# Performance work log

Measured on AMD Instinct MI355X. Metric: run time of the kernel, lower is better.

## Reference

```python
import jax, jax.numpy as jnp
import numpy as np

N_NODES = 100000
N_EDGES = 1600000
IN_FEATS, HIDDEN, N_CLASSES = 128, 64, 16


def setup_inputs() -> dict:
    key = jax.random.key(0)
    ks = jax.random.split(key, 10)
    feats = jax.random.normal(ks[0], (N_NODES, IN_FEATS), dtype=jnp.float32)
    src = jax.random.randint(ks[1], (N_EDGES,), 0, N_NODES, dtype=jnp.int32)
    dst = jax.random.randint(ks[2], (N_EDGES,), 0, N_NODES, dtype=jnp.int32)
    def glorot(k, fan_in, fan_out):
        lim = np.sqrt(6.0 / (fan_in + fan_out)).astype(np.float32)
        return jax.random.uniform(k, (fan_in, fan_out), jnp.float32, -lim, lim)
    return {
        "features": feats, "src": src, "dst": dst,
        "W0": glorot(ks[3], IN_FEATS, HIDDEN), "b0": jnp.zeros((HIDDEN,), jnp.float32),
        "W1": glorot(ks[4], HIDDEN, HIDDEN), "b1": jnp.zeros((HIDDEN,), jnp.float32),
        "W2": glorot(ks[5], HIDDEN, N_CLASSES), "b2": jnp.zeros((N_CLASSES,), jnp.float32),
    }


def _graph_conv(src, dst, x, W, b, act):
    # DGL GraphConv, norm='both': out = D_in^{-1/2} A (D_out^{-1/2} x) W + b
    n = x.shape[0]
    ones = jnp.ones((src.shape[0],), x.dtype)
    deg_out = jnp.clip(jax.ops.segment_sum(ones, src, num_segments=n), 1.0)
    deg_in = jnp.clip(jax.ops.segment_sum(ones, dst, num_segments=n), 1.0)
    # DGL applies W first when in_dim > out_dim (same math, less edge traffic)
    pre = x.shape[1] > W.shape[1]
    h = x @ W if pre else x
    h = h * jax.lax.rsqrt(deg_out)[:, None]
    agg = jax.ops.segment_sum(h[src], dst, num_segments=n)  # [N, d]
    agg = agg * jax.lax.rsqrt(deg_in)[:, None]
    out = (agg if pre else agg @ W) + b
    return act(out) if act is not None else out


def reference(features, src, dst, W0, b0, W1, b1, W2, b2):
    relu = jax.nn.relu
    h = _graph_conv(src, dst, features, W0, b0, relu)
    h = _graph_conv(src, dst, h, W1, b1, relu)        # dropout p=0.0 -> identity
    h = _graph_conv(src, dst, h, W2, b2, None)
    return h
```

## Files before the change

### kernel.cpp

```cpp
#include <hip/hip_runtime.h>

#define NN 100000
#define NE 1600000
#define NBUCK 782
#define PCHUNK 4096
#define HISTB 256
#define NREP 8
#define STAGE_CAP 12288

struct alignas(8) US4 { unsigned short x, y, z, w; };

__device__ __forceinline__ float bfu(unsigned int hw) { return __uint_as_float(hw << 16); }
__device__ __forceinline__ unsigned short f2bf(float f) {
    unsigned int u = __float_as_uint(f);
    return (unsigned short)((u + 0x7fffu + ((u >> 16) & 1u)) >> 16);
}


__global__ __launch_bounds__(256) void k_hist(const int* __restrict__ src,
                                              const int* __restrict__ dst,
                                              int* __restrict__ bcnt8_d,
                                              int* __restrict__ bcnt8_s) {
    __shared__ int hd[NBUCK], hs[NBUCK];
    int tid = threadIdx.x;
    for (int i = tid; i < NBUCK; i += 256) { hd[i] = 0; hs[i] = 0; }
    __syncthreads();
    int* md = bcnt8_d + (size_t)(blockIdx.x & (NREP - 1)) * NBUCK;
    int* ms = bcnt8_s + (size_t)(blockIdx.x & (NREP - 1)) * NBUCK;
    int stride = gridDim.x * 256;
    for (int e = blockIdx.x * 256 + tid; e < NE; e += stride) {
        atomicAdd(&hd[dst[e] >> 7], 1);
        atomicAdd(&hs[src[e] >> 7], 1);
    }
    __syncthreads();
    for (int i = tid; i < NBUCK; i += 256) {
        if (hd[i]) atomicAdd(&md[i], hd[i]);
        if (hs[i]) atomicAdd(&ms[i], hs[i]);
    }
}

__global__ __launch_bounds__(1024) void k_bscan(const int* __restrict__ bcnt8_d,
                                                const int* __restrict__ bcnt8_s,
                                                int* __restrict__ base_d,
                                                int* __restrict__ cursor_d,
                                                int* __restrict__ base_s,
                                                int* __restrict__ cursor_s,
                                                unsigned short* __restrict__ A,
                                                unsigned short* __restrict__ B,
                                                unsigned short* __restrict__ C16,
                                                int* __restrict__ EBg) {
    if (blockIdx.x == 2) {
        int t = threadIdx.x;
        if (t < 64) {
            A[(size_t)NN * 64 + t] = 0;
            B[(size_t)NN * 64 + t] = 0;
        }
        if (t < 16) {
            C16[(size_t)NN * 16 + t] = 0;
            EBg[NE + t] = NN;
        }
        return;
    }
    __shared__ int tmp[1024];
    int t = threadIdx.x;
    const int* bc = blockIdx.x ? bcnt8_s : bcnt8_d;
    int* base = blockIdx.x ? base_s : base_d;
    int* cur = blockIdx.x ? cursor_s : cursor_d;
    int v = 0;
    if (t < NBUCK)
#pragma unroll
        for (int c = 0; c < NREP; ++c) v += bc[c * NBUCK + t];
    tmp[t] = v;
    __syncthreads();
    for (int off = 1; off < 1024; off <<= 1) {
        int u = (t >= off) ? tmp[t - off] : 0;
        __syncthreads();
        tmp[t] += u;
        __syncthreads();
    }
    int excl = tmp[t] - v;
    if (t < NBUCK) {
        base[t] = excl;
        cur[t] = excl;
    }
    if (t == 0) base[NBUCK] = NE;
}

__global__ __launch_bounds__(256) void k_pairs(const int* __restrict__ src,
                                               const int* __restrict__ dst,
                                               int* __restrict__ cursor_d,
                                               int* __restrict__ cursor_s,
                                               int* __restrict__ E2d,
                                               unsigned char* __restrict__ E2s) {
    __shared__ int hist_d[NBUCK], gbase_d[NBUCK], hist_s[NBUCK], gbase_s[NBUCK];
    int tid = threadIdx.x;
    for (int i = tid; i < NBUCK; i += 256) { hist_d[i] = 0; hist_s[i] = 0; }
    __syncthreads();
    int base = blockIdx.x * PCHUNK;
#pragma unroll
    for (int i = 0; i < PCHUNK / 256; ++i) {
        int e = base + i * 256 + tid;
        if (e < NE) {
            atomicAdd(&hist_d[dst[e] >> 7], 1);
            atomicAdd(&hist_s[src[e] >> 7], 1);
        }
    }
    __syncthreads();
    int rot = (int)((blockIdx.x * 191u) % NBUCK);
    for (int ii = tid; ii < NBUCK; ii += 256) {
        int i = ii + rot;
        if (i >= NBUCK) i -= NBUCK;
        int h = hist_d[i];
        if (h) gbase_d[i] = atomicAdd(&cursor_d[i], h);
        hist_d[i] = 0;
        h = hist_s[i];
        if (h) gbase_s[i] = atomicAdd(&cursor_s[i], h);
        hist_s[i] = 0;
    }
    __syncthreads();
#pragma unroll
    for (int i = 0; i < PCHUNK / 256; ++i) {
        int e = base + i * 256 + tid;
        if (e < NE) {
            int s = src[e], d = dst[e];
            int bd = d >> 7;
            int pd = atomicAdd(&hist_d[bd], 1);
            E2d[gbase_d[bd] + pd] = (s << 7) | (d & 127);
            int bs = s >> 7;
            int ps = atomicAdd(&hist_s[bs], 1);
            E2s[gbase_s[bs] + ps] = (unsigned char)(s & 127);
        }
    }
}

__global__ __launch_bounds__(256) void k_nodes(int* __restrict__ EB,
                                               const int* __restrict__ base_d,
                                               const unsigned char* __restrict__ E2s,
                                               const int* __restrict__ base_s,
                                               int* __restrict__ rowdesc,
                                               float* __restrict__ r_in,
                                               float* __restrict__ r_out) {
    __shared__ int cnt[128], cur[128];
    __shared__ int stage[STAGE_CAP];
    int tid = threadIdx.x;
    int b = blockIdx.x;
    if (b >= NBUCK) {
        b -= NBUCK;
        int base = base_s[b], end = base_s[b + 1];
        if (tid < 128) cnt[tid] = 0;
        __syncthreads();
        for (int i = base + tid; i < end; i += 256) atomicAdd(&cnt[E2s[i]], 1);
        __syncthreads();
        if (tid < 128) {
            int node = b * 128 + tid;
            if (node < NN) r_out[node] = rsqrtf((float)max(cnt[tid], 1));
        }
        return;
    }
    int base = base_d[b], end = base_d[b + 1];
    int m = min(end - base, STAGE_CAP);
    if (tid < 128) cnt[tid] = 0;
    __syncthreads();
    for (int i = tid; i < m; i += 256) {
        int e = EB[base + i];
        stage[i] = e;
        atomicAdd(&cnt[e & 127], 1);
    }
    __syncthreads();
    int v = (tid < 128) ? cnt[tid] : 0;
    for (int off = 1; off < 128; off <<= 1) {
        int u = (tid >= off && tid < 128) ? cnt[tid - off] : 0;
        __syncthreads();
        if (tid < 128) cnt[tid] += u;
        __syncthreads();
    }
    if (tid < 128) {
        int excl = cnt[tid] - v;
        cur[tid] = excl;
        int node = b * 128 + tid;
        if (node < NN) {
            rowdesc[node] = ((base + excl) << 9) | min(v, 511);
            r_in[node] = rsqrtf((float)max(v, 1));
        }
    }
    __syncthreads();
    for (int i = tid; i < m; i += 256) {
        int e = stage[i];
        int pos = atomicAdd(&cur[e & 127], 1);
        EB[base + pos] = e >> 7;
    }
}


__global__ __launch_bounds__(256) void k_gemm0(const float* __restrict__ x,
                                               const float* __restrict__ W0,
                                               const float* __restrict__ r_out,
                                               unsigned short* __restrict__ A) {
    __shared__ float xl[64 * 129];
    __shared__ float wl[64 * 64];
    int tid = threadIdx.x;
    int m0 = blockIdx.x * 64;
#pragma unroll
    for (int i = 0; i < 8; ++i) {
        int idx = i * 256 + tid;
        int m = idx >> 5, kc = idx & 31;
        int gm = min(m0 + m, NN - 1);
        float4 v = *(const float4*)&x[(size_t)gm * 128 + kc * 4];
        float* p = &xl[m * 129 + kc * 4];
        p[0] = v.x; p[1] = v.y; p[2] = v.z; p[3] = v.w;
    }
    int tn = tid & 15, tm = tid >> 4;
    float acc[4][4] = {};
    const float4* W4 = (const float4*)W0;
    float4* wl4 = (float4*)wl;
    for (int h = 0; h < 2; ++h) {
        __syncthreads();
#pragma unroll
        for (int i = 0; i < 4; ++i) wl4[i * 256 + tid] = W4[h * 1024 + i * 256 + tid];
        __syncthreads();
#pragma unroll 4
        for (int k = 0; k < 64; ++k) {
            int kk = h * 64 + k;
            float4 wv = *(const float4*)&wl[k * 64 + tn * 4];
            float xv[4];
#pragma unroll
            for (int i = 0; i < 4; ++i) xv[i] = xl[(tm * 4 + i) * 129 + kk];
#pragma unroll
            for (int i = 0; i < 4; ++i) {
                acc[i][0] = fmaf(xv[i], wv.x, acc[i][0]);
                acc[i][1] = fmaf(xv[i], wv.y, acc[i][1]);
                acc[i][2] = fmaf(xv[i], wv.z, acc[i][2]);
                acc[i][3] = fmaf(xv[i], wv.w, acc[i][3]);
            }
        }
    }
#pragma unroll
    for (int i = 0; i < 4; ++i) {
        int m = m0 + tm * 4 + i;
        if (m < NN) {
            float ro = r_out[m];
            US4 o = {f2bf(acc[i][0] * ro), f2bf(acc[i][1] * ro),
                     f2bf(acc[i][2] * ro), f2bf(acc[i][3] * ro)};
            *(US4*)&A[(size_t)m * 64 + tn * 4] = o;
        }
    }
}

__global__ __launch_bounds__(256) void k_mlp(const unsigned short* __restrict__ G,
                                             const float* __restrict__ W1,
                                             const float* __restrict__ b1,
                                             const float* __restrict__ W2,
                                             const float* __restrict__ r_out,
                                             unsigned short* __restrict__ C16) {
    __shared__ float gl[64 * 65];
    __shared__ float w1l[64 * 64];
    __shared__ float w2l[64 * 16];
    int tid = threadIdx.x;
    int m0 = blockIdx.x * 64;
#pragma unroll
    for (int i = 0; i < 2; ++i) {
        int idx = i * 256 + tid;
        int m = idx >> 3, c8 = idx & 7;
        int gm = min(m0 + m, NN - 1);
        uint4 u = *(const uint4*)&G[(size_t)gm * 64 + c8 * 8];
        float* p = &gl[m * 65 + c8 * 8];
        p[0] = bfu(u.x & 0xffffu); p[1] = bfu(u.x >> 16);
        p[2] = bfu(u.y & 0xffffu); p[3] = bfu(u.y >> 16);
        p[4] = bfu(u.z & 0xffffu); p[5] = bfu(u.z >> 16);
        p[6] = bfu(u.w & 0xffffu); p[7] = bfu(u.w >> 16);
    }
    float4* w1l4 = (float4*)w1l;
    const float4* W1_4 = (const float4*)W1;
#pragma unroll
    for (int i = 0; i < 4; ++i) w1l4[i * 256 + tid] = W1_4[i * 256 + tid];
    ((float4*)w2l)[tid] = ((const float4*)W2)[tid];
    __syncthreads();
    int tn = tid & 15, tm = tid >> 4;
    float acc[4][4] = {};
#pragma unroll 4
    for (int k = 0; k < 64; ++k) {
        float4 wv = *(const float4*)&w1l[k * 64 + tn * 4];
        float xv[4];
#pragma unroll
        for (int i = 0; i < 4; ++i) xv[i] = gl[(tm * 4 + i) * 65 + k];
#pragma unroll
        for (int i = 0; i < 4; ++i) {
            acc[i][0] = fmaf(xv[i], wv.x, acc[i][0]);
            acc[i][1] = fmaf(xv[i], wv.y, acc[i][1]);
            acc[i][2] = fmaf(xv[i], wv.z, acc[i][2]);
            acc[i][3] = fmaf(xv[i], wv.w, acc[i][3]);
        }
    }
    float4 bb = *(const float4*)&b1[tn * 4];
    __syncthreads();
#pragma unroll
    for (int i = 0; i < 4; ++i) {
        gl[(tm * 4 + i) * 65 + tn * 4 + 0] = fmaxf(acc[i][0] + bb.x, 0.f);
        gl[(tm * 4 + i) * 65 + tn * 4 + 1] = fmaxf(acc[i][1] + bb.y, 0.f);
        gl[(tm * 4 + i) * 65 + tn * 4 + 2] = fmaxf(acc[i][2] + bb.z, 0.f);
        gl[(tm * 4 + i) * 65 + tn * 4 + 3] = fmaxf(acc[i][3] + bb.w, 0.f);
    }
    __syncthreads();
    int m = tid >> 2, n0 = (tid & 3) * 4;
    float a2[4] = {};
#pragma unroll 8
    for (int k = 0; k < 64; ++k) {
        float zv = gl[m * 65 + k];
        float4 wv = *(const float4*)&w2l[k * 16 + n0];
        a2[0] = fmaf(zv, wv.x, a2[0]);
        a2[1] = fmaf(zv, wv.y, a2[1]);
        a2[2] = fmaf(zv, wv.z, a2[2]);
        a2[3] = fmaf(zv, wv.w, a2[3]);
    }
    int node = m0 + m;
    if (node < NN) {
        float ro = r_out[node];
        US4 o = {f2bf(a2[0] * ro), f2bf(a2[1] * ro), f2bf(a2[2] * ro), f2bf(a2[3] * ro)};
        *(US4*)&C16[(size_t)node * 16 + n0] = o;
    }
}


template <int MODE>
__global__ __launch_bounds__(256) void k_gb64(const int* __restrict__ rowdesc,
                                              const int* __restrict__ csr,
                                              const unsigned short* __restrict__ h,
                                              const float* __restrict__ r_in,
                                              const float* __restrict__ r_out,
                                              const float* __restrict__ bias,
                                              unsigned short* __restrict__ o16) {
    int tid = threadIdx.x;
    int wave = tid >> 6, lane = tid & 63;
    int n0 = (blockIdx.x * 4 + wave) * 2, n1 = n0 + 1;
    int rdA = rowdesc[n0], rdB = rowdesc[n1];
    int jbA = rdA >> 9, degA = rdA & 511;
    int jbB = rdB >> 9, degB = rdB & 511;
    int itn = max((degA + 7) >> 3, (degB + 7) >> 3);
    int g = lane >> 3, f8 = lane & 7;
    const int* cA = csr + jbA + g;
    const int* cB = csr + jbB + g;
    const unsigned short* hp = h + f8 * 8;
    float aA[8] = {}, aB[8] = {};
    for (int it = 0; it < itn; it += 2) {
        int s0 = it * 8 + g, s1 = s0 + 8;
        int eA0 = cA[it * 8];
        int eA1 = cA[it * 8 + 8];
        int eB0 = cB[it * 8];
        int eB1 = cB[it * 8 + 8];
        eA0 = (s0 < degA) ? eA0 : NN;
        eA1 = (s1 < degA) ? eA1 : NN;
        eB0 = (s0 < degB) ? eB0 : NN;
        eB1 = (s1 < degB) ? eB1 : NN;
        uint4 u0 = *(const uint4*)(hp + (size_t)eA0 * 64);
        uint4 u1 = *(const uint4*)(hp + (size_t)eA1 * 64);
        uint4 u2 = *(const uint4*)(hp + (size_t)eB0 * 64);
        uint4 u3 = *(const uint4*)(hp + (size_t)eB1 * 64);
        aA[0] += bfu(u0.x & 0xffffu); aA[1] += bfu(u0.x >> 16);
        aA[2] += bfu(u0.y & 0xffffu); aA[3] += bfu(u0.y >> 16);
        aA[4] += bfu(u0.z & 0xffffu); aA[5] += bfu(u0.z >> 16);
        aA[6] += bfu(u0.w & 0xffffu); aA[7] += bfu(u0.w >> 16);
        aA[0] += bfu(u1.x & 0xffffu); aA[1] += bfu(u1.x >> 16);
        aA[2] += bfu(u1.y & 0xffffu); aA[3] += bfu(u1.y >> 16);
        aA[4] += bfu(u1.z & 0xffffu); aA[5] += bfu(u1.z >> 16);
        aA[6] += bfu(u1.w & 0xffffu); aA[7] += bfu(u1.w >> 16);
        aB[0] += bfu(u2.x & 0xffffu); aB[1] += bfu(u2.x >> 16);
        aB[2] += bfu(u2.y & 0xffffu); aB[3] += bfu(u2.y >> 16);
        aB[4] += bfu(u2.z & 0xffffu); aB[5] += bfu(u2.z >> 16);
        aB[6] += bfu(u2.w & 0xffffu); aB[7] += bfu(u2.w >> 16);
        aB[0] += bfu(u3.x & 0xffffu); aB[1] += bfu(u3.x >> 16);
        aB[2] += bfu(u3.y & 0xffffu); aB[3] += bfu(u3.y >> 16);
        aB[4] += bfu(u3.z & 0xffffu); aB[5] += bfu(u3.z >> 16);
        aB[6] += bfu(u3.w & 0xffffu); aB[7] += bfu(u3.w >> 16);
    }
#pragma unroll
    for (int m = 8; m <= 32; m <<= 1) {
#pragma unroll
        for (int k = 0; k < 8; ++k) {
            aA[k] += __shfl_xor(aA[k], m);
            aB[k] += __shfl_xor(aB[k], m);
        }
    }
    if (g < 2) {
        int nw = g ? n1 : n0;
        float o[8];
#pragma unroll
        for (int k = 0; k < 8; ++k) o[k] = g ? aB[k] : aA[k];
        float ri = r_in[nw];
        unsigned short ov[8];
        if (MODE == 0) {
            float ro = r_out[nw];
            float4 bA = *(const float4*)&bias[f8 * 8];
            float4 bB = *(const float4*)&bias[f8 * 8 + 4];
            float bb[8] = {bA.x, bA.y, bA.z, bA.w, bB.x, bB.y, bB.z, bB.w};
#pragma unroll
            for (int k = 0; k < 8; ++k)
                ov[k] = f2bf(fmaxf(fmaf(o[k], ri, bb[k]), 0.f) * ro);
        } else {
#pragma unroll
            for (int k = 0; k < 8; ++k) ov[k] = f2bf(o[k] * ri);
        }
        uint4 ow;
        ow.x = (unsigned)ov[0] | ((unsigned)ov[1] << 16);
        ow.y = (unsigned)ov[2] | ((unsigned)ov[3] << 16);
        ow.z = (unsigned)ov[4] | ((unsigned)ov[5] << 16);
        ow.w = (unsigned)ov[6] | ((unsigned)ov[7] << 16);
        *(uint4*)&o16[(size_t)nw * 64 + f8 * 8] = ow;
    }
}

__global__ __launch_bounds__(256) void k_gb16(const int* __restrict__ rowdesc,
                                              const int* __restrict__ csr,
                                              const unsigned short* __restrict__ C16,
                                              const float* __restrict__ r_in,
                                              const float* __restrict__ b2,
                                              float* __restrict__ out) {
    int tid = threadIdx.x;
    int wave = tid >> 6, lane = tid & 63;
    int n0 = (blockIdx.x * 4 + wave) * 2, n1 = n0 + 1;
    int rdA = rowdesc[n0], rdB = rowdesc[n1];
    int jbA = rdA >> 9, degA = rdA & 511;
    int jbB = rdB >> 9, degB = rdB & 511;
    int itn = max((degA + 7) >> 3, (degB + 7) >> 3);
    int g = lane >> 3, p = lane & 7;
    const int* cA = csr + jbA + g;
    const int* cB = csr + jbB + g;
    const unsigned short* cp = C16 + p * 2;
    float a0A = 0.f, a1A = 0.f, a0B = 0.f, a1B = 0.f;
    for (int it = 0; it < itn; it += 2) {
        int s0 = it * 8 + g, s1 = s0 + 8;
        int eA0 = cA[it * 8];
        int eA1 = cA[it * 8 + 8];
        int eB0 = cB[it * 8];
        int eB1 = cB[it * 8 + 8];
        eA0 = (s0 < degA) ? eA0 : NN;
        eA1 = (s1 < degA) ? eA1 : NN;
        eB0 = (s0 < degB) ? eB0 : NN;
        eB1 = (s1 < degB) ? eB1 : NN;
        unsigned u0 = *(const unsigned*)(cp + (size_t)eA0 * 16);
        unsigned u1 = *(const unsigned*)(cp + (size_t)eA1 * 16);
        unsigned u2 = *(const unsigned*)(cp + (size_t)eB0 * 16);
        unsigned u3 = *(const unsigned*)(cp + (size_t)eB1 * 16);
        a0A += bfu(u0 & 0xffffu); a1A += bfu(u0 >> 16);
        a0A += bfu(u1 & 0xffffu); a1A += bfu(u1 >> 16);
        a0B += bfu(u2 & 0xffffu); a1B += bfu(u2 >> 16);
        a0B += bfu(u3 & 0xffffu); a1B += bfu(u3 >> 16);
    }
#pragma unroll
    for (int m = 8; m <= 32; m <<= 1) {
        a0A += __shfl_xor(a0A, m);
        a1A += __shfl_xor(a1A, m);
        a0B += __shfl_xor(a0B, m);
        a1B += __shfl_xor(a1B, m);
    }
    if (g < 2) {
        int nw = g ? n1 : n0;
        float x0 = g ? a0B : a0A;
        float x1 = g ? a1B : a1A;
        float ri = r_in[nw];
        float2 bb = *(const float2*)&b2[p * 2];
        float2 o;
        o.x = fmaf(x0, ri, bb.x);
        o.y = fmaf(x1, ri, bb.y);
        *(float2*)&out[(size_t)nw * 16 + p * 2] = o;
    }
}

extern "C" void kernel_launch(void* const* d_in, const int* in_sizes, int n_in,
                              void* d_out, int out_size, void* d_ws, size_t ws_size,
                              hipStream_t stream) {
    const float* feats = (const float*)d_in[0];
    const int* src = (const int*)d_in[1];
    const int* dst = (const int*)d_in[2];
    const float* W0 = (const float*)d_in[3];
    const float* b0 = (const float*)d_in[4];
    const float* W1 = (const float*)d_in[5];
    const float* b1 = (const float*)d_in[6];
    const float* W2 = (const float*)d_in[7];
    const float* b2 = (const float*)d_in[8];
    float* out = (float*)d_out;

    float* ws = (float*)d_ws;
    float* r_out = ws;
    float* r_in = ws + NN;
    int* rowdesc = (int*)(ws + 2 * NN);
    int* EB = (int*)(ws + 3 * NN);
    unsigned char* E2s = (unsigned char*)(ws + 3 * NN + NE + 16);
    float* R1 = ws + 3 * NN + NE + 16 + NE / 4;
    float* R2 = R1 + (size_t)32 * (NN + 1);
    float* Creg = R2 + (size_t)32 * (NN + 1);
    int* base_d = (int*)(Creg + (size_t)8 * (NN + 1));
    int* cursor_d = base_d + NBUCK + 1;
    int* base_s = cursor_d + NBUCK;
    int* cursor_s = base_s + NBUCK + 1;
    int* bcnt8_d = cursor_s + NBUCK;
    int* bcnt8_s = bcnt8_d + NREP * NBUCK;

    unsigned short* A = (unsigned short*)R1;
    unsigned short* G = A;
    unsigned short* B = (unsigned short*)R2;
    unsigned short* C16 = (unsigned short*)Creg;

    hipMemsetAsync(bcnt8_d, 0, 2 * NREP * NBUCK * sizeof(int), stream);
    k_hist<<<HISTB, 256, 0, stream>>>(src, dst, bcnt8_d, bcnt8_s);
    k_bscan<<<3, 1024, 0, stream>>>(bcnt8_d, bcnt8_s, base_d, cursor_d, base_s, cursor_s,
                                    A, B, C16, EB);
    k_pairs<<<(NE + PCHUNK - 1) / PCHUNK, 256, 0, stream>>>(src, dst, cursor_d, cursor_s,
                                                            EB, E2s);
    k_nodes<<<2 * NBUCK, 256, 0, stream>>>(EB, base_d, E2s, base_s, rowdesc, r_in, r_out);

    k_gemm0<<<(NN + 63) / 64, 256, 0, stream>>>(feats, W0, r_out, A);
    k_gb64<0><<<NN / 8, 256, 0, stream>>>(rowdesc, EB, A, r_in, r_out, b0, B);

    k_gb64<1><<<NN / 8, 256, 0, stream>>>(rowdesc, EB, B, r_in, r_out, b0, G);
    k_mlp<<<(NN + 63) / 64, 256, 0, stream>>>(G, W1, b1, W2, r_out, C16);

    k_gb16<<<NN / 8, 256, 0, stream>>>(rowdesc, EB, C16, r_in, b2, out);
}
```

Measured before the change: 342.2 us.

## Split 64-wide gather aggregation into two 32-feature half passes

The 64-feature bf16 gather-sum kernel now handles half of the feature columns per launch. Each of the two launches has a wave process four destination nodes with 16 edge groups of 4 lanes, instead of two nodes with 8 groups of 8 lanes. Halving the gathered working set per pass is meant to improve cache hit rates on the random row gathers and to raise memory-level parallelism. In exchange the CSR indices are read twice, there are extra launches, and each gather is 16 bytes out of a 128-byte row.

```diff
diff --git a/kernel.cpp b/kernel.cpp
--- a/kernel.cpp
+++ b/kernel.cpp
@@ -322,76 +322,86 @@
 
 
 template <int MODE>
-__global__ __launch_bounds__(256) void k_gb64(const int* __restrict__ rowdesc,
-                                              const int* __restrict__ csr,
-                                              const unsigned short* __restrict__ h,
-                                              const float* __restrict__ r_in,
-                                              const float* __restrict__ r_out,
-                                              const float* __restrict__ bias,
-                                              unsigned short* __restrict__ o16) {
+__global__ __launch_bounds__(256) void k_gb64h(const int* __restrict__ rowdesc,
+                                               const int* __restrict__ csr,
+                                               const unsigned short* __restrict__ h,
+                                               const float* __restrict__ r_in,
+                                               const float* __restrict__ r_out,
+                                               const float* __restrict__ bias,
+                                               int fo,
+                                               unsigned short* __restrict__ o16) {
     int tid = threadIdx.x;
     int wave = tid >> 6, lane = tid & 63;
-    int n0 = (blockIdx.x * 4 + wave) * 2, n1 = n0 + 1;
-    int rdA = rowdesc[n0], rdB = rowdesc[n1];
+    int n0 = (blockIdx.x * 4 + wave) * 4;
+    int rdA = rowdesc[n0], rdB = rowdesc[n0 + 1];
+    int rdC = rowdesc[n0 + 2], rdD = rowdesc[n0 + 3];
     int jbA = rdA >> 9, degA = rdA & 511;
     int jbB = rdB >> 9, degB = rdB & 511;
-    int itn = max((degA + 7) >> 3, (degB + 7) >> 3);
-    int g = lane >> 3, f8 = lane & 7;
+    int jbC = rdC >> 9, degC = rdC & 511;
+    int jbD = rdD >> 9, degD = rdD & 511;
+    int itn = max(max((degA + 15) >> 4, (degB + 15) >> 4),
+                  max((degC + 15) >> 4, (degD + 15) >> 4));
+    int g = lane >> 2, f4 = lane & 3;
     const int* cA = csr + jbA + g;
     const int* cB = csr + jbB + g;
-    const unsigned short* hp = h + f8 * 8;
-    float aA[8] = {}, aB[8] = {};
-    for (int it = 0; it < itn; it += 2) {
-        int s0 = it * 8 + g, s1 = s0 + 8;
-        int eA0 = cA[it * 8];
-        int eA1 = cA[it * 8 + 8];
-        int eB0 = cB[it * 8];
-        int eB1 = cB[it * 8 + 8];
-        eA0 = (s0 < degA) ? eA0 : NN;
-        eA1 = (s1 < degA) ? eA1 : NN;
-        eB0 = (s0 < degB) ? eB0 : NN;
-        eB1 = (s1 < degB) ? eB1 : NN;
-        uint4 u0 = *(const uint4*)(hp + (size_t)eA0 * 64);
-        uint4 u1 = *(const uint4*)(hp + (size_t)eA1 * 64);
-        uint4 u2 = *(const uint4*)(hp + (size_t)eB0 * 64);
-        uint4 u3 = *(const uint4*)(hp + (size_t)eB1 * 64);
-        aA[0] += bfu(u0.x & 0xffffu); aA[1] += bfu(u0.x >> 16);
-        aA[2] += bfu(u0.y & 0xffffu); aA[3] += bfu(u0.y >> 16);
-        aA[4] += bfu(u0.z & 0xffffu); aA[5] += bfu(u0.z >> 16);
-        aA[6] += bfu(u0.w & 0xffffu); aA[7] += bfu(u0.w >> 16);
-        aA[0] += bfu(u1.x & 0xffffu); aA[1] += bfu(u1.x >> 16);
-        aA[2] += bfu(u1.y & 0xffffu); aA[3] += bfu(u1.y >> 16);
-        aA[4] += bfu(u1.z & 0xffffu); aA[5] += bfu(u1.z >> 16);
-        aA[6] += bfu(u1.w & 0xffffu); aA[7] += bfu(u1.w >> 16);
-        aB[0] += bfu(u2.x & 0xffffu); aB[1] += bfu(u2.x >> 16);
-        aB[2] += bfu(u2.y & 0xffffu); aB[3] += bfu(u2.y >> 16);
-        aB[4] += bfu(u2.z & 0xffffu); aB[5] += bfu(u2.z >> 16);
-        aB[6] += bfu(u2.w & 0xffffu); aB[7] += bfu(u2.w >> 16);
-        aB[0] += bfu(u3.x & 0xffffu); aB[1] += bfu(u3.x >> 16);
-        aB[2] += bfu(u3.y & 0xffffu); aB[3] += bfu(u3.y >> 16);
-        aB[4] += bfu(u3.z & 0xffffu); aB[5] += bfu(u3.z >> 16);
-        aB[6] += bfu(u3.w & 0xffffu); aB[7] += bfu(u3.w >> 16);
-    }
-#pragma unroll
-    for (int m = 8; m <= 32; m <<= 1) {
+    const int* cC = csr + jbC + g;
+    const int* cD = csr + jbD + g;
+    const unsigned short* hp = h + fo + f4 * 8;
+    float aA[8] = {}, aB[8] = {}, aC[8] = {}, aD[8] = {};
+    for (int it = 0; it < itn; ++it) {
+        int s = it * 16 + g;
+        int eA = cA[it * 16];
+        int eB = cB[it * 16];
+        int eC = cC[it * 16];
+        int eD = cD[it * 16];
+        eA = (s < degA) ? eA : NN;
+        eB = (s < degB) ? eB : NN;
+        eC = (s < degC) ? eC : NN;
+        eD = (s < degD) ? eD : NN;
+        uint4 uA = *(const uint4*)(hp + (size_t)eA * 64);
+        uint4 uB = *(const uint4*)(hp + (size_t)eB * 64);
+        uint4 uC = *(const uint4*)(hp + (size_t)eC * 64);
+        uint4 uD = *(const uint4*)(hp + (size_t)eD * 64);
+        aA[0] += bfu(uA.x & 0xffffu); aA[1] += bfu(uA.x >> 16);
+        aA[2] += bfu(uA.y & 0xffffu); aA[3] += bfu(uA.y >> 16);
+        aA[4] += bfu(uA.z & 0xffffu); aA[5] += bfu(uA.z >> 16);
+        aA[6] += bfu(uA.w & 0xffffu); aA[7] += bfu(uA.w >> 16);
+        aB[0] += bfu(uB.x & 0xffffu); aB[1] += bfu(uB.x >> 16);
+        aB[2] += bfu(uB.y & 0xffffu); aB[3] += bfu(uB.y >> 16);
+        aB[4] += bfu(uB.z & 0xffffu); aB[5] += bfu(uB.z >> 16);
+        aB[6] += bfu(uB.w & 0xffffu); aB[7] += bfu(uB.w >> 16);
+        aC[0] += bfu(uC.x & 0xffffu); aC[1] += bfu(uC.x >> 16);
+        aC[2] += bfu(uC.y & 0xffffu); aC[3] += bfu(uC.y >> 16);
+        aC[4] += bfu(uC.z & 0xffffu); aC[5] += bfu(uC.z >> 16);
+        aC[6] += bfu(uC.w & 0xffffu); aC[7] += bfu(uC.w >> 16);
+        aD[0] += bfu(uD.x & 0xffffu); aD[1] += bfu(uD.x >> 16);
+        aD[2] += bfu(uD.y & 0xffffu); aD[3] += bfu(uD.y >> 16);
+        aD[4] += bfu(uD.z & 0xffffu); aD[5] += bfu(uD.z >> 16);
+        aD[6] += bfu(uD.w & 0xffffu); aD[7] += bfu(uD.w >> 16);
+    }
+#pragma unroll
+    for (int m = 4; m <= 32; m <<= 1) {
 #pragma unroll
         for (int k = 0; k < 8; ++k) {
             aA[k] += __shfl_xor(aA[k], m);
             aB[k] += __shfl_xor(aB[k], m);
-        }
-    }
-    if (g < 2) {
-        int nw = g ? n1 : n0;
+            aC[k] += __shfl_xor(aC[k], m);
+            aD[k] += __shfl_xor(aD[k], m);
+        }
+    }
+    if (g < 4) {
+        int nw = n0 + g;
         float o[8];
 #pragma unroll
-        for (int k = 0; k < 8; ++k) o[k] = g ? aB[k] : aA[k];
+        for (int k = 0; k < 8; ++k)
+            o[k] = (g == 0) ? aA[k] : (g == 1) ? aB[k] : (g == 2) ? aC[k] : aD[k];
         float ri = r_in[nw];
         unsigned short ov[8];
         if (MODE == 0) {
             float ro = r_out[nw];
-            float4 bA = *(const float4*)&bias[f8 * 8];
-            float4 bB = *(const float4*)&bias[f8 * 8 + 4];
-            float bb[8] = {bA.x, bA.y, bA.z, bA.w, bB.x, bB.y, bB.z, bB.w};
+            float4 b0v = *(const float4*)&bias[fo + f4 * 8];
+            float4 b1v = *(const float4*)&bias[fo + f4 * 8 + 4];
+            float bb[8] = {b0v.x, b0v.y, b0v.z, b0v.w, b1v.x, b1v.y, b1v.z, b1v.w};
 #pragma unroll
             for (int k = 0; k < 8; ++k)
                 ov[k] = f2bf(fmaxf(fmaf(o[k], ri, bb[k]), 0.f) * ro);
@@ -404,7 +414,7 @@
         ow.y = (unsigned)ov[2] | ((unsigned)ov[3] << 16);
         ow.z = (unsigned)ov[4] | ((unsigned)ov[5] << 16);
         ow.w = (unsigned)ov[6] | ((unsigned)ov[7] << 16);
-        *(uint4*)&o16[(size_t)nw * 64 + f8 * 8] = ow;
+        *(uint4*)&o16[(size_t)nw * 64 + fo + f4 * 8] = ow;
     }
 }
 
@@ -509,9 +519,11 @@
     k_nodes<<<2 * NBUCK, 256, 0, stream>>>(EB, base_d, E2s, base_s, rowdesc, r_in, r_out);
 
     k_gemm0<<<(NN + 63) / 64, 256, 0, stream>>>(feats, W0, r_out, A);
-    k_gb64<0><<<NN / 8, 256, 0, stream>>>(rowdesc, EB, A, r_in, r_out, b0, B);
-
-    k_gb64<1><<<NN / 8, 256, 0, stream>>>(rowdesc, EB, B, r_in, r_out, b0, G);
+    k_gb64h<0><<<NN / 16, 256, 0, stream>>>(rowdesc, EB, A, r_in, r_out, b0, 0, B);
+    k_gb64h<0><<<NN / 16, 256, 0, stream>>>(rowdesc, EB, A, r_in, r_out, b0, 32, B);
+
+    k_gb64h<1><<<NN / 16, 256, 0, stream>>>(rowdesc, EB, B, r_in, r_out, b0, 0, G);
+    k_gb64h<1><<<NN / 16, 256, 0, stream>>>(rowdesc, EB, B, r_in, r_out, b0, 32, G);
     k_mlp<<<(NN + 63) / 64, 256, 0, stream>>>(G, W1, b1, W2, r_out, C16);
 
     k_gb16<<<NN / 8, 256, 0, stream>>>(rowdesc, EB, C16, r_in, b2, out);
```

After: 410.9 us. 1.2x slower.

## Compute out-degree via global atomics in histogram pass, drop source bucketing

Applied to the files above, without the earlier changes.

Out-degrees are now counted directly with global atomics into 8 replicated per-node arrays during the histogram pass, then reduced in extra blocks of the scan kernel to produce r_out. This removes the source-side bucket scatter (E2s), its cursor and scan, and half of the k_nodes grid. k_pairs also moves to 8192-edge chunks with 512 threads. The trade is scattered global atomics over 100k nodes and a larger memset in place of the LDS-based bucket path.

```diff
diff --git a/kernel.cpp b/kernel.cpp
--- a/kernel.cpp
+++ b/kernel.cpp
@@ -3,7 +3,7 @@
 #define NN 100000
 #define NE 1600000
 #define NBUCK 782
-#define PCHUNK 4096
+#define PCHUNK 8192
 #define HISTB 256
 #define NREP 8
 #define STAGE_CAP 12288
@@ -20,37 +20,35 @@
 __global__ __launch_bounds__(256) void k_hist(const int* __restrict__ src,
                                               const int* __restrict__ dst,
                                               int* __restrict__ bcnt8_d,
-                                              int* __restrict__ bcnt8_s) {
-    __shared__ int hd[NBUCK], hs[NBUCK];
-    int tid = threadIdx.x;
-    for (int i = tid; i < NBUCK; i += 256) { hd[i] = 0; hs[i] = 0; }
+                                              int* __restrict__ deg8) {
+    __shared__ int hd[NBUCK];
+    int tid = threadIdx.x;
+    for (int i = tid; i < NBUCK; i += 256) hd[i] = 0;
     __syncthreads();
     int* md = bcnt8_d + (size_t)(blockIdx.x & (NREP - 1)) * NBUCK;
-    int* ms = bcnt8_s + (size_t)(blockIdx.x & (NREP - 1)) * NBUCK;
+    int* dg = deg8 + (size_t)(blockIdx.x & (NREP - 1)) * NN;
     int stride = gridDim.x * 256;
     for (int e = blockIdx.x * 256 + tid; e < NE; e += stride) {
         atomicAdd(&hd[dst[e] >> 7], 1);
-        atomicAdd(&hs[src[e] >> 7], 1);
+        atomicAdd(&dg[src[e]], 1);
     }
     __syncthreads();
     for (int i = tid; i < NBUCK; i += 256) {
         if (hd[i]) atomicAdd(&md[i], hd[i]);
-        if (hs[i]) atomicAdd(&ms[i], hs[i]);
     }
 }
 
 __global__ __launch_bounds__(1024) void k_bscan(const int* __restrict__ bcnt8_d,
-                                                const int* __restrict__ bcnt8_s,
                                                 int* __restrict__ base_d,
                                                 int* __restrict__ cursor_d,
-                                                int* __restrict__ base_s,
-                                                int* __restrict__ cursor_s,
+                                                const int* __restrict__ deg8,
+                                                float* __restrict__ r_out,
                                                 unsigned short* __restrict__ A,
                                                 unsigned short* __restrict__ B,
                                                 unsigned short* __restrict__ C16,
                                                 int* __restrict__ EBg) {
-    if (blockIdx.x == 2) {
-        int t = threadIdx.x;
+    int t = threadIdx.x;
+    if (blockIdx.x == 1) {
         if (t < 64) {
             A[(size_t)NN * 64 + t] = 0;
             B[(size_t)NN * 64 + t] = 0;
@@ -61,15 +59,21 @@
         }
         return;
     }
+    if (blockIdx.x >= 2) {
+        int node = (blockIdx.x - 2) * 1024 + t;
+        if (node < NN) {
+            int d = 0;
+#pragma unroll
+            for (int c = 0; c < NREP; ++c) d += deg8[(size_t)c * NN + node];
+            r_out[node] = rsqrtf((float)max(d, 1));
+        }
+        return;
+    }
     __shared__ int tmp[1024];
-    int t = threadIdx.x;
-    const int* bc = blockIdx.x ? bcnt8_s : bcnt8_d;
-    int* base = blockIdx.x ? base_s : base_d;
-    int* cur = blockIdx.x ? cursor_s : cursor_d;
     int v = 0;
     if (t < NBUCK)
 #pragma unroll
-        for (int c = 0; c < NREP; ++c) v += bc[c * NBUCK + t];
+        for (int c = 0; c < NREP; ++c) v += bcnt8_d[c * NBUCK + t];
     tmp[t] = v;
     __syncthreads();
     for (int off = 1; off < 1024; off <<= 1) {
@@ -80,83 +84,56 @@
     }
     int excl = tmp[t] - v;
     if (t < NBUCK) {
-        base[t] = excl;
-        cur[t] = excl;
-    }
-    if (t == 0) base[NBUCK] = NE;
-}
-
-__global__ __launch_bounds__(256) void k_pairs(const int* __restrict__ src,
+        base_d[t] = excl;
+        cursor_d[t] = excl;
+    }
+    if (t == 0) base_d[NBUCK] = NE;
+}
+
+__global__ __launch_bounds__(512) void k_pairs(const int* __restrict__ src,
                                                const int* __restrict__ dst,
                                                int* __restrict__ cursor_d,
-                                               int* __restrict__ cursor_s,
-                                               int* __restrict__ E2d,
-                                               unsigned char* __restrict__ E2s) {
-    __shared__ int hist_d[NBUCK], gbase_d[NBUCK], hist_s[NBUCK], gbase_s[NBUCK];
-    int tid = threadIdx.x;
-    for (int i = tid; i < NBUCK; i += 256) { hist_d[i] = 0; hist_s[i] = 0; }
+                                               int* __restrict__ E2d) {
+    __shared__ int hist_d[NBUCK], gbase_d[NBUCK];
+    int tid = threadIdx.x;
+    for (int i = tid; i < NBUCK; i += 512) hist_d[i] = 0;
     __syncthreads();
     int base = blockIdx.x * PCHUNK;
 #pragma unroll
-    for (int i = 0; i < PCHUNK / 256; ++i) {
-        int e = base + i * 256 + tid;
-        if (e < NE) {
-            atomicAdd(&hist_d[dst[e] >> 7], 1);
-            atomicAdd(&hist_s[src[e] >> 7], 1);
-        }
+    for (int i = 0; i < PCHUNK / 512; ++i) {
+        int e = base + i * 512 + tid;
+        if (e < NE) atomicAdd(&hist_d[dst[e] >> 7], 1);
     }
     __syncthreads();
     int rot = (int)((blockIdx.x * 191u) % NBUCK);
-    for (int ii = tid; ii < NBUCK; ii += 256) {
+    for (int ii = tid; ii < NBUCK; ii += 512) {
         int i = ii + rot;
         if (i >= NBUCK) i -= NBUCK;
         int h = hist_d[i];
         if (h) gbase_d[i] = atomicAdd(&cursor_d[i], h);
         hist_d[i] = 0;
-        h = hist_s[i];
-        if (h) gbase_s[i] = atomicAdd(&cursor_s[i], h);
-        hist_s[i] = 0;
-    }
-    __syncthreads();
-#pragma unroll
-    for (int i = 0; i < PCHUNK / 256; ++i) {
-        int e = base + i * 256 + tid;
+    }
+    __syncthreads();
+#pragma unroll
+    for (int i = 0; i < PCHUNK / 512; ++i) {
+        int e = base + i * 512 + tid;
         if (e < NE) {
             int s = src[e], d = dst[e];
             int bd = d >> 7;
             int pd = atomicAdd(&hist_d[bd], 1);
             E2d[gbase_d[bd] + pd] = (s << 7) | (d & 127);
-            int bs = s >> 7;
-            int ps = atomicAdd(&hist_s[bs], 1);
-            E2s[gbase_s[bs] + ps] = (unsigned char)(s & 127);
         }
     }
 }
 
 __global__ __launch_bounds__(256) void k_nodes(int* __restrict__ EB,
                                                const int* __restrict__ base_d,
-                                               const unsigned char* __restrict__ E2s,
-                                               const int* __restrict__ base_s,
                                                int* __restrict__ rowdesc,
-                                               float* __restrict__ r_in,
-                                               float* __restrict__ r_out) {
+                                               float* __restrict__ r_in) {
     __shared__ int cnt[128], cur[128];
     __shared__ int stage[STAGE_CAP];
     int tid = threadIdx.x;
     int b = blockIdx.x;
-    if (b >= NBUCK) {
-        b -= NBUCK;
-        int base = base_s[b], end = base_s[b + 1];
-        if (tid < 128) cnt[tid] = 0;
-        __syncthreads();
-        for (int i = base + tid; i < end; i += 256) atomicAdd(&cnt[E2s[i]], 1);
-        __syncthreads();
-        if (tid < 128) {
-            int node = b * 128 + tid;
-            if (node < NN) r_out[node] = rsqrtf((float)max(cnt[tid], 1));
-        }
-        return;
-    }
     int base = base_d[b], end = base_d[b + 1];
     int m = min(end - base, STAGE_CAP);
     if (tid < 128) cnt[tid] = 0;
@@ -484,29 +461,25 @@
     float* r_in = ws + NN;
     int* rowdesc = (int*)(ws + 2 * NN);
     int* EB = (int*)(ws + 3 * NN);
-    unsigned char* E2s = (unsigned char*)(ws + 3 * NN + NE + 16);
-    float* R1 = ws + 3 * NN + NE + 16 + NE / 4;
+    float* R1 = ws + 3 * NN + NE + 16;
     float* R2 = R1 + (size_t)32 * (NN + 1);
     float* Creg = R2 + (size_t)32 * (NN + 1);
     int* base_d = (int*)(Creg + (size_t)8 * (NN + 1));
     int* cursor_d = base_d + NBUCK + 1;
-    int* base_s = cursor_d + NBUCK;
-    int* cursor_s = base_s + NBUCK + 1;
-    int* bcnt8_d = cursor_s + NBUCK;
-    int* bcnt8_s = bcnt8_d + NREP * NBUCK;
+    int* bcnt8_d = cursor_d + NBUCK;
+    int* deg8 = bcnt8_d + NREP * NBUCK;
 
     unsigned short* A = (unsigned short*)R1;
     unsigned short* G = A;
     unsigned short* B = (unsigned short*)R2;
     unsigned short* C16 = (unsigned short*)Creg;
 
-    hipMemsetAsync(bcnt8_d, 0, 2 * NREP * NBUCK * sizeof(int), stream);
-    k_hist<<<HISTB, 256, 0, stream>>>(src, dst, bcnt8_d, bcnt8_s);
-    k_bscan<<<3, 1024, 0, stream>>>(bcnt8_d, bcnt8_s, base_d, cursor_d, base_s, cursor_s,
-                                    A, B, C16, EB);
-    k_pairs<<<(NE + PCHUNK - 1) / PCHUNK, 256, 0, stream>>>(src, dst, cursor_d, cursor_s,
-                                                            EB, E2s);
-    k_nodes<<<2 * NBUCK, 256, 0, stream>>>(EB, base_d, E2s, base_s, rowdesc, r_in, r_out);
+    hipMemsetAsync(bcnt8_d, 0, (size_t)(NREP * NBUCK + NREP * NN) * sizeof(int), stream);
+    k_hist<<<HISTB, 256, 0, stream>>>(src, dst, bcnt8_d, deg8);
+    k_bscan<<<2 + (NN + 1023) / 1024, 1024, 0, stream>>>(bcnt8_d, base_d, cursor_d, deg8,
+                                                         r_out, A, B, C16, EB);
+    k_pairs<<<(NE + PCHUNK - 1) / PCHUNK, 512, 0, stream>>>(src, dst, cursor_d, EB);
+    k_nodes<<<NBUCK, 256, 0, stream>>>(EB, base_d, rowdesc, r_in);
 
     k_gemm0<<<(NN + 63) / 64, 256, 0, stream>>>(feats, W0, r_out, A);
     k_gb64<0><<<NN / 8, 256, 0, stream>>>(rowdesc, EB, A, r_in, r_out, b0, B);
```

After: 367.1 us. +7.3%, slower.
